# Kernel optimization log

Hardware: AMD Instinct MI355X
Metric: run time of the kernel (lower is better)

The kernel has to match this reference:

```python
import jax, jax.numpy as jnp
import numpy as np

B, L, V, E, H = 64, 256, 256, 256, 1024

def setup_inputs() -> dict:
    key = jax.random.key(0)
    ks = jax.random.split(key, 7)
    inputs = jax.random.randint(ks[0], (B, L), 0, V, dtype=jnp.int32)
    embedding = jax.random.normal(ks[1], (V, E), dtype=jnp.float32)  # stddev=1.0 per emb_init
    # GRU weights: input projections (no bias) and hidden projections (with bias),
    # concatenated over gates [r, z, n].
    Wi = jax.random.normal(ks[2], (E, 3 * H), dtype=jnp.float32) / np.sqrt(E)
    Wh = jax.random.normal(ks[3], (H, 3 * H), dtype=jnp.float32) / np.sqrt(H)
    bh = jnp.zeros((3 * H,), dtype=jnp.float32)
    # Output dense (xavier_uniform-like scale)
    lim = np.sqrt(6.0 / (H + V))
    Wout = jax.random.uniform(ks[4], (H, V), dtype=jnp.float32, minval=-lim, maxval=lim)
    bout = jax.random.normal(ks[5], (V,), dtype=jnp.float32) * 1e-6
    return {"inputs": inputs, "embedding": embedding, "Wi": Wi, "Wh": Wh,
            "bh": bh, "Wout": Wout, "bout": bout}

def reference(inputs, embedding, Wi, Wh, bh, Wout, bout):
    # Embedding lookup: [B, L] -> [B, L, E]
    x = jnp.take(embedding, inputs, axis=0)
    # Precompute input-side gate projections for all timesteps (batched GEMM).
    xw = jnp.einsum('ble,ef->blf', x, Wi)  # [B, L, 3H]
    hidden = Wh.shape[0]

    def step(h, xw_t):
        gh = h @ Wh + bh                       # [B, 3H]
        xr, xz, xn = jnp.split(xw_t, 3, axis=-1)
        hr, hz, hn = jnp.split(gh, 3, axis=-1)
        r = jax.nn.sigmoid(xr + hr)
        z = jax.nn.sigmoid(xz + hz)
        n = jnp.tanh(xn + r * hn)
        h_new = (1.0 - z) * n + z * h          # GRUCell update
        return h_new, h_new

    h0 = jnp.zeros((x.shape[0], hidden), dtype=x.dtype)
    _, ys = jax.lax.scan(step, h0, jnp.swapaxes(xw, 0, 1))  # scan over time
    y = jnp.swapaxes(ys, 0, 1)                 # [B, L, H]
    logits = jnp.einsum('blh,hv->blv', y, Wout) + bout
    return logits
```

## Files before the change

### kernel.cpp

```cpp
#include <hip/hip_runtime.h>
#include <cstdint>
#include <math.h>

#define B_  64
#define L_  256
#define V_  256
#define E_  256
#define H_  1024
#define H3  3072

typedef __bf16 bf16x8 __attribute__((ext_vector_type(8)));
typedef float  f32x4  __attribute__((ext_vector_type(4)));

__device__ __forceinline__ unsigned short f2bf(float f) {
    union { float f; unsigned u; } v; v.f = f;
    unsigned r = v.u + 0x7fffu + ((v.u >> 16) & 1u);
    return (unsigned short)(r >> 16);
}
__device__ __forceinline__ float bf2f(unsigned short u) {
    union { unsigned u; float f; } v; v.u = ((unsigned)u) << 16;
    return v.f;
}

__device__ __forceinline__ int chunk_ok(bf16x8 v) {
    union { bf16x8 b; unsigned u[4]; } cv; cv.b = v;
    int ok = 1;
#pragma unroll
    for (int i = 0; i < 4; i++) {
        unsigned x = cv.u[i] ^ 0xAAAAAAAAu;
        ok &= (int)((x & 0xFFFFu) != 0u) & (int)((x >> 16) != 0u);
    }
    return ok;
}

__global__ __launch_bounds__(256) void prep_transpose_tiled(const float* __restrict__ src,
                                                            unsigned short* __restrict__ dst,
                                                            int rows, int cols) {
    __shared__ unsigned short tile[32][34];
    int n0 = blockIdx.x * 32;
    int k0 = blockIdx.y * 32;
    int tx = threadIdx.x & 31, ty = threadIdx.x >> 5;
#pragma unroll
    for (int j = 0; j < 32; j += 8) {
        float v = src[(size_t)(k0 + ty + j) * cols + (n0 + tx)];
        tile[tx][ty + j] = f2bf(v);
    }
    __syncthreads();
#pragma unroll
    for (int j = 0; j < 32; j += 8)
        dst[(size_t)(n0 + ty + j) * rows + (k0 + tx)] = tile[ty + j][tx];
}

__global__ __launch_bounds__(256) void poison_hist(uint4* __restrict__ p) {
    size_t T = (size_t)blockIdx.x * 256 + threadIdx.x;
    uint4 v; v.x = v.y = v.z = v.w = 0xAAAAAAAAu;
#pragma unroll
    for (int k = 0; k < 4; k++) p[T + (size_t)k * 524288] = v;
}

__global__ void prep_misc(const float* __restrict__ emb,
                          unsigned short* __restrict__ embB,
                          unsigned short* __restrict__ h0b) {
    int idx = blockIdx.x * 256 + threadIdx.x;
    embB[idx] = f2bf(emb[idx]);
    h0b[idx]  = 0;
}

__global__ __launch_bounds__(256, 1) void gru_persistent(
        unsigned short* __restrict__ hist,
        const unsigned short* __restrict__ WhT,
        const unsigned short* __restrict__ WiT,
        const unsigned short* __restrict__ embB,
        const int* __restrict__ tokens,
        const float* __restrict__ bh,
        unsigned short* __restrict__ yB) {
    __shared__ f32x4 red[2][4][6][64];

    int bid = blockIdx.x;
    int btile = bid & 3;
    int jtile = bid >> 2;
    int wave = threadIdx.x >> 6, lane = threadIdx.x & 63;
    int l16 = lane & 15, q = lane >> 4;
    int b0 = btile * 16, j0 = jtile * 16;
    int kbase = wave * 256;

    bf16x8 Wreg[3][8];
#pragma unroll
    for (int g = 0; g < 3; g++) {
        const bf16x8* Brow = (const bf16x8*)(WhT + (size_t)(g * H_ + j0 + l16) * H_);
#pragma unroll
        for (int kk = 0; kk < 8; kk++) {
            Wreg[g][kk] = Brow[(kbase >> 3) + kk * 4 + q];
            asm volatile("" : "+v"(Wreg[g][kk]));
        }
    }
    bf16x8 Wxreg[3][2];
#pragma unroll
    for (int g = 0; g < 3; g++) {
        const bf16x8* Bx = (const bf16x8*)(WiT + (size_t)(g * H_ + j0 + l16) * E_);
#pragma unroll
        for (int c = 0; c < 2; c++) {
            Wxreg[g][c] = Bx[wave * 8 + c * 4 + q];
            asm volatile("" : "+v"(Wxreg[g][c]));
        }
    }

    int Lp  = threadIdx.x & 63;
    int reg = threadIdx.x >> 6;
    int b_local = (Lp >> 4) * 4 + reg;
    int j_local = Lp & 15;
    int b = b0 + b_local, jg = j0 + j_local;
    float bhr = bh[jg];
    float bhz = bh[H_ + jg];
    float bhn = bh[2 * H_ + jg];
    asm volatile("" : "+v"(bhr), "+v"(bhz), "+v"(bhn));
    float hreg = 0.0f;

    const int tokrow = (b0 + l16) * L_;

    for (int t = 0; t < L_; t++) {
        const unsigned short* hist_t  = hist + (size_t)t * (B_ * H_);
        unsigned short*       hist_t1 = hist + (size_t)(t + 1) * (B_ * H_);

        int tok = tokens[tokrow + t];
        const bf16x8* Ax = (const bf16x8*)(embB + (size_t)tok * E_);
        bf16x8 ax0 = Ax[wave * 8 + q];
        bf16x8 ax1 = Ax[wave * 8 + 4 + q];
        f32x4 xacc[3] = {};
#pragma unroll
        for (int g = 0; g < 3; g++) {
            xacc[g] = __builtin_amdgcn_mfma_f32_16x16x32_bf16(ax0, Wxreg[g][0], xacc[g], 0, 0, 0);
            xacc[g] = __builtin_amdgcn_mfma_f32_16x16x32_bf16(ax1, Wxreg[g][1], xacc[g], 0, 0, 0);
        }

        const unsigned short* p = hist_t + (size_t)(b0 + l16) * H_ + kbase + q * 8;
        bf16x8 a0, a1, a2, a3, a4, a5, a6, a7;
        while (true) {
            asm volatile("global_load_dwordx4 %0, %1, off sc0 sc1" : "=v"(a0) : "v"(p));
            asm volatile("global_load_dwordx4 %0, %1, off sc0 sc1" : "=v"(a1) : "v"(p + 32));
            asm volatile("global_load_dwordx4 %0, %1, off sc0 sc1" : "=v"(a2) : "v"(p + 64));
            asm volatile("global_load_dwordx4 %0, %1, off sc0 sc1" : "=v"(a3) : "v"(p + 96));
            asm volatile("global_load_dwordx4 %0, %1, off sc0 sc1" : "=v"(a4) : "v"(p + 128));
            asm volatile("global_load_dwordx4 %0, %1, off sc0 sc1" : "=v"(a5) : "v"(p + 160));
            asm volatile("global_load_dwordx4 %0, %1, off sc0 sc1" : "=v"(a6) : "v"(p + 192));
            asm volatile("global_load_dwordx4 %0, %1, off sc0 sc1" : "=v"(a7) : "v"(p + 224));
            asm volatile("s_waitcnt vmcnt(0)"
                         : "+v"(a0), "+v"(a1), "+v"(a2), "+v"(a3),
                           "+v"(a4), "+v"(a5), "+v"(a6), "+v"(a7)
                         :: "memory");
            int ok = chunk_ok(a0) & chunk_ok(a1) & chunk_ok(a2) & chunk_ok(a3)
                   & chunk_ok(a4) & chunk_ok(a5) & chunk_ok(a6) & chunk_ok(a7);
            if (__all(ok)) break;
            __builtin_amdgcn_s_sleep(1);
        }

        f32x4 acc[3] = {};
#pragma unroll
        for (int g = 0; g < 3; g++) {
            acc[g] = __builtin_amdgcn_mfma_f32_16x16x32_bf16(a0, Wreg[g][0], acc[g], 0, 0, 0);
            acc[g] = __builtin_amdgcn_mfma_f32_16x16x32_bf16(a1, Wreg[g][1], acc[g], 0, 0, 0);
            acc[g] = __builtin_amdgcn_mfma_f32_16x16x32_bf16(a2, Wreg[g][2], acc[g], 0, 0, 0);
            acc[g] = __builtin_amdgcn_mfma_f32_16x16x32_bf16(a3, Wreg[g][3], acc[g], 0, 0, 0);
            acc[g] = __builtin_amdgcn_mfma_f32_16x16x32_bf16(a4, Wreg[g][4], acc[g], 0, 0, 0);
            acc[g] = __builtin_amdgcn_mfma_f32_16x16x32_bf16(a5, Wreg[g][5], acc[g], 0, 0, 0);
            acc[g] = __builtin_amdgcn_mfma_f32_16x16x32_bf16(a6, Wreg[g][6], acc[g], 0, 0, 0);
            acc[g] = __builtin_amdgcn_mfma_f32_16x16x32_bf16(a7, Wreg[g][7], acc[g], 0, 0, 0);
        }

        int par = t & 1;
#pragma unroll
        for (int g = 0; g < 3; g++) {
            red[par][wave][g][lane]     = acc[g];
            red[par][wave][3 + g][lane] = xacc[g];
        }
        __syncthreads();

        float gh0 = red[par][0][0][Lp][reg] + red[par][1][0][Lp][reg] + red[par][2][0][Lp][reg] + red[par][3][0][Lp][reg];
        float gh1 = red[par][0][1][Lp][reg] + red[par][1][1][Lp][reg] + red[par][2][1][Lp][reg] + red[par][3][1][Lp][reg];
        float gh2 = red[par][0][2][Lp][reg] + red[par][1][2][Lp][reg] + red[par][2][2][Lp][reg] + red[par][3][2][Lp][reg];
        float xr  = red[par][0][3][Lp][reg] + red[par][1][3][Lp][reg] + red[par][2][3][Lp][reg] + red[par][3][3][Lp][reg];
        float xz  = red[par][0][4][Lp][reg] + red[par][1][4][Lp][reg] + red[par][2][4][Lp][reg] + red[par][3][4][Lp][reg];
        float xn  = red[par][0][5][Lp][reg] + red[par][1][5][Lp][reg] + red[par][2][5][Lp][reg] + red[par][3][5][Lp][reg];

        float r = 1.0f / (1.0f + __expf(-(xr + gh0 + bhr)));
        float z = 1.0f / (1.0f + __expf(-(xz + gh1 + bhz)));
        float n = tanhf(xn + r * (gh2 + bhn));
        float hnew = (1.0f - z) * n + z * hreg;
        hreg = hnew;

        unsigned short hbv = f2bf(hnew);
        if (hbv == 0xAAAAu) hbv = 0xAAABu;

        {
            unsigned short* hp = hist_t1 + (size_t)b * H_ + jg;
            unsigned hv32 = hbv;
            asm volatile("global_store_short %0, %1, off sc0 sc1"
                         :: "v"(hp), "v"(hv32) : "memory");
        }
        yB[((size_t)b * L_ + t) * H_ + jg] = hbv;
    }
}

__global__ __launch_bounds__(256) void out_gemm(const unsigned short* __restrict__ yB,
                                                const unsigned short* __restrict__ WoutT,
                                                const float* __restrict__ bout,
                                                float* __restrict__ out) {
    int ntile = blockIdx.x;
    int mtile = blockIdx.y;
    int wave = threadIdx.x >> 6, lane = threadIdx.x & 63;
    int l16 = lane & 15, q = lane >> 4;

    int m = mtile * 64 + wave * 16 + l16;
    const bf16x8* Arow = (const bf16x8*)(yB + (size_t)m * H_);
    int n0 = ntile * 64;

    f32x4 acc[4] = {};
    for (int k0 = 0; k0 < H_; k0 += 32) {
        bf16x8 a = Arow[(k0 >> 3) + q];
#pragma unroll
        for (int j = 0; j < 4; j++) {
            const bf16x8* Brow = (const bf16x8*)(WoutT + (size_t)(n0 + j*16 + l16) * H_);
            bf16x8 b = Brow[(k0 >> 3) + q];
            acc[j] = __builtin_amdgcn_mfma_f32_16x16x32_bf16(a, b, acc[j], 0, 0, 0);
        }
    }
    int mrow = mtile * 64 + wave * 16 + q * 4;
#pragma unroll
    for (int j = 0; j < 4; j++) {
        int n = n0 + j * 16 + l16;
        float bias = bout[n];
#pragma unroll
        for (int r = 0; r < 4; r++)
            out[(size_t)(mrow + r) * V_ + n] = acc[j][r] + bias;
    }
}

extern "C" void kernel_launch(void* const* d_in, const int* in_sizes, int n_in,
                              void* d_out, int out_size, void* d_ws, size_t ws_size,
                              hipStream_t stream) {
    const int*   tokens = (const int*)  d_in[0];
    const float* emb    = (const float*)d_in[1];
    const float* Wi     = (const float*)d_in[2];
    const float* Wh     = (const float*)d_in[3];
    const float* bh     = (const float*)d_in[4];
    const float* Wout   = (const float*)d_in[5];
    const float* bout   = (const float*)d_in[6];
    float* out = (float*)d_out;

    char* ws = (char*)d_ws;
    size_t off = 0;
    auto alloc = [&](size_t bytes) -> void* {
        void* p = ws + off;
        off += (bytes + 255) & ~(size_t)255;
        return p;
    };
    unsigned short* WhT   = (unsigned short*)alloc((size_t)H3 * H_ * 2);
    unsigned short* WiT   = (unsigned short*)alloc((size_t)H3 * E_ * 2);
    unsigned short* WoutT = (unsigned short*)alloc((size_t)V_ * H_ * 2);
    unsigned short* embB  = (unsigned short*)alloc((size_t)V_ * E_ * 2);
    unsigned short* yB    = (unsigned short*)alloc((size_t)B_ * L_ * H_ * 2);
    unsigned short* hist  = (unsigned short*)alloc((size_t)(L_ + 1) * B_ * H_ * 2);

    prep_transpose_tiled<<<dim3(H3 / 32, H_ / 32), 256, 0, stream>>>(Wh, WhT, H_, H3);
    prep_transpose_tiled<<<dim3(H3 / 32, E_ / 32), 256, 0, stream>>>(Wi, WiT, E_, H3);
    prep_transpose_tiled<<<dim3(V_ / 32, H_ / 32), 256, 0, stream>>>(Wout, WoutT, H_, V_);
    poison_hist<<<2048, 256, 0, stream>>>((uint4*)(hist + (size_t)B_ * H_));
    prep_misc<<<(V_ * E_) / 256, 256, 0, stream>>>(emb, embB, hist);

    {
        unsigned short* ah = hist;
        const unsigned short* aW = WhT; const unsigned short* aWx = WiT;
        const unsigned short* ae = embB; const int* at = tokens;
        const float* ab = bh; unsigned short* ay = yB;
        void* args[] = {&ah, &aW, &aWx, &ae, &at, &ab, &ay};
        hipLaunchCooperativeKernel((void*)gru_persistent, dim3(256), dim3(256),
                                   args, 0, stream);
    }

    out_gemm<<<dim3(4, 256), 256, 0, stream>>>(yB, WoutT, bout, out);
}
```

Before: 992.9 us.

## Replace poisoned history polling with per-block step flags and double-buffered hidden state

Drops the full per-timestep hidden-state history and the kernel that filled it with a poison pattern. In their place come two ping-pong hidden buffers and per-block progress flags. After storing its hidden slice, each block drains its stores, syncs and publishes its step counter; before reading, wave 0 spins until all 64 column blocks in its batch group have reached the step. This removes the large poison write and the repeated poll-and-validate reloads of the history. In exchange it adds a store drain, an extra block barrier and a flag round trip to each step's critical path, and the spin has a timeout that could silently break ordering.

New measurement: 1.053 ms. 1.06x slower.

```diff
diff --git a/kernel.cpp b/kernel.cpp
--- a/kernel.cpp
+++ b/kernel.cpp
@@ -16,21 +16,6 @@
     union { float f; unsigned u; } v; v.f = f;
     unsigned r = v.u + 0x7fffu + ((v.u >> 16) & 1u);
     return (unsigned short)(r >> 16);
-}
-__device__ __forceinline__ float bf2f(unsigned short u) {
-    union { unsigned u; float f; } v; v.u = ((unsigned)u) << 16;
-    return v.f;
-}
-
-__device__ __forceinline__ int chunk_ok(bf16x8 v) {
-    union { bf16x8 b; unsigned u[4]; } cv; cv.b = v;
-    int ok = 1;
-#pragma unroll
-    for (int i = 0; i < 4; i++) {
-        unsigned x = cv.u[i] ^ 0xAAAAAAAAu;
-        ok &= (int)((x & 0xFFFFu) != 0u) & (int)((x >> 16) != 0u);
-    }
-    return ok;
 }
 
 __global__ __launch_bounds__(256) void prep_transpose_tiled(const float* __restrict__ src,
@@ -51,29 +36,26 @@
         dst[(size_t)(n0 + ty + j) * rows + (k0 + tx)] = tile[ty + j][tx];
 }
 
-__global__ __launch_bounds__(256) void poison_hist(uint4* __restrict__ p) {
-    size_t T = (size_t)blockIdx.x * 256 + threadIdx.x;
-    uint4 v; v.x = v.y = v.z = v.w = 0xAAAAAAAAu;
-#pragma unroll
-    for (int k = 0; k < 4; k++) p[T + (size_t)k * 524288] = v;
-}
-
 __global__ void prep_misc(const float* __restrict__ emb,
                           unsigned short* __restrict__ embB,
-                          unsigned short* __restrict__ h0b) {
+                          unsigned short* __restrict__ h0b,
+                          unsigned* __restrict__ flags) {
     int idx = blockIdx.x * 256 + threadIdx.x;
     embB[idx] = f2bf(emb[idx]);
     h0b[idx]  = 0;
+    if (idx < 4096) flags[idx] = 0;
 }
 
 __global__ __launch_bounds__(256, 1) void gru_persistent(
-        unsigned short* __restrict__ hist,
+        unsigned short* __restrict__ hbuf0,
+        unsigned short* __restrict__ hbuf1,
         const unsigned short* __restrict__ WhT,
         const unsigned short* __restrict__ WiT,
         const unsigned short* __restrict__ embB,
         const int* __restrict__ tokens,
         const float* __restrict__ bh,
-        unsigned short* __restrict__ yB) {
+        unsigned short* __restrict__ yB,
+        unsigned* __restrict__ flagp) {
     __shared__ f32x4 red[2][4][6][64];
 
     int bid = blockIdx.x;
@@ -83,6 +65,9 @@
     int l16 = lane & 15, q = lane >> 4;
     int b0 = btile * 16, j0 = jtile * 16;
     int kbase = wave * 256;
+
+    unsigned* grpflags = flagp + (btile << 10);
+    unsigned* myflag   = grpflags + (jtile << 4);
 
     bf16x8 Wreg[3][8];
 #pragma unroll
@@ -118,9 +103,11 @@
 
     const int tokrow = (b0 + l16) * L_;
 
+    unsigned short* hcur = hbuf0;
+    unsigned short* hnxt = hbuf1;
+
     for (int t = 0; t < L_; t++) {
-        const unsigned short* hist_t  = hist + (size_t)t * (B_ * H_);
-        unsigned short*       hist_t1 = hist + (size_t)(t + 1) * (B_ * H_);
+        int par = t & 1;
 
         int tok = tokens[tokrow + t];
         const bf16x8* Ax = (const bf16x8*)(embB + (size_t)tok * E_);
@@ -133,26 +120,36 @@
             xacc[g] = __builtin_amdgcn_mfma_f32_16x16x32_bf16(ax1, Wxreg[g][1], xacc[g], 0, 0, 0);
         }
 
-        const unsigned short* p = hist_t + (size_t)(b0 + l16) * H_ + kbase + q * 8;
+        if (t > 0) {
+            if (wave == 0) {
+                unsigned tgt = (unsigned)t;
+                int spins = 0;
+                while (true) {
+                    unsigned f = __hip_atomic_load(grpflags + (lane << 4),
+                                                   __ATOMIC_RELAXED,
+                                                   __HIP_MEMORY_SCOPE_AGENT);
+                    if (__all((int)(f >= tgt))) break;
+                    if (++spins > (1 << 20)) break;
+                    __builtin_amdgcn_s_sleep(1);
+                }
+            }
+            __syncthreads();
+        }
+
+        const unsigned short* p = hcur + (size_t)(b0 + l16) * H_ + kbase + q * 8;
         bf16x8 a0, a1, a2, a3, a4, a5, a6, a7;
-        while (true) {
-            asm volatile("global_load_dwordx4 %0, %1, off sc0 sc1" : "=v"(a0) : "v"(p));
-            asm volatile("global_load_dwordx4 %0, %1, off sc0 sc1" : "=v"(a1) : "v"(p + 32));
-            asm volatile("global_load_dwordx4 %0, %1, off sc0 sc1" : "=v"(a2) : "v"(p + 64));
-            asm volatile("global_load_dwordx4 %0, %1, off sc0 sc1" : "=v"(a3) : "v"(p + 96));
-            asm volatile("global_load_dwordx4 %0, %1, off sc0 sc1" : "=v"(a4) : "v"(p + 128));
-            asm volatile("global_load_dwordx4 %0, %1, off sc0 sc1" : "=v"(a5) : "v"(p + 160));
-            asm volatile("global_load_dwordx4 %0, %1, off sc0 sc1" : "=v"(a6) : "v"(p + 192));
-            asm volatile("global_load_dwordx4 %0, %1, off sc0 sc1" : "=v"(a7) : "v"(p + 224));
-            asm volatile("s_waitcnt vmcnt(0)"
-                         : "+v"(a0), "+v"(a1), "+v"(a2), "+v"(a3),
-                           "+v"(a4), "+v"(a5), "+v"(a6), "+v"(a7)
-                         :: "memory");
-            int ok = chunk_ok(a0) & chunk_ok(a1) & chunk_ok(a2) & chunk_ok(a3)
-                   & chunk_ok(a4) & chunk_ok(a5) & chunk_ok(a6) & chunk_ok(a7);
-            if (__all(ok)) break;
-            __builtin_amdgcn_s_sleep(1);
-        }
+        asm volatile("global_load_dwordx4 %0, %1, off sc0 sc1" : "=v"(a0) : "v"(p));
+        asm volatile("global_load_dwordx4 %0, %1, off sc0 sc1" : "=v"(a1) : "v"(p + 32));
+        asm volatile("global_load_dwordx4 %0, %1, off sc0 sc1" : "=v"(a2) : "v"(p + 64));
+        asm volatile("global_load_dwordx4 %0, %1, off sc0 sc1" : "=v"(a3) : "v"(p + 96));
+        asm volatile("global_load_dwordx4 %0, %1, off sc0 sc1" : "=v"(a4) : "v"(p + 128));
+        asm volatile("global_load_dwordx4 %0, %1, off sc0 sc1" : "=v"(a5) : "v"(p + 160));
+        asm volatile("global_load_dwordx4 %0, %1, off sc0 sc1" : "=v"(a6) : "v"(p + 192));
+        asm volatile("global_load_dwordx4 %0, %1, off sc0 sc1" : "=v"(a7) : "v"(p + 224));
+        asm volatile("s_waitcnt vmcnt(0)"
+                     : "+v"(a0), "+v"(a1), "+v"(a2), "+v"(a3),
+                       "+v"(a4), "+v"(a5), "+v"(a6), "+v"(a7)
+                     :: "memory");
 
         f32x4 acc[3] = {};
 #pragma unroll
@@ -166,8 +163,6 @@
             acc[g] = __builtin_amdgcn_mfma_f32_16x16x32_bf16(a6, Wreg[g][6], acc[g], 0, 0, 0);
             acc[g] = __builtin_amdgcn_mfma_f32_16x16x32_bf16(a7, Wreg[g][7], acc[g], 0, 0, 0);
         }
-
-        int par = t & 1;
 #pragma unroll
         for (int g = 0; g < 3; g++) {
             red[par][wave][g][lane]     = acc[g];
@@ -189,15 +184,22 @@
         hreg = hnew;
 
         unsigned short hbv = f2bf(hnew);
-        if (hbv == 0xAAAAu) hbv = 0xAAABu;
-
         {
-            unsigned short* hp = hist_t1 + (size_t)b * H_ + jg;
+            unsigned short* hp = hnxt + (size_t)b * H_ + jg;
             unsigned hv32 = hbv;
             asm volatile("global_store_short %0, %1, off sc0 sc1"
                          :: "v"(hp), "v"(hv32) : "memory");
         }
+        asm volatile("s_waitcnt vmcnt(0)" ::: "memory");
+        __syncthreads();
+
+        if (threadIdx.x == 0)
+            __hip_atomic_store(myflag, (unsigned)(t + 1), __ATOMIC_RELAXED,
+                               __HIP_MEMORY_SCOPE_AGENT);
+
         yB[((size_t)b * L_ + t) * H_ + jg] = hbv;
+
+        unsigned short* tmp = hcur; hcur = hnxt; hnxt = tmp;
     }
 }
 
@@ -259,22 +261,28 @@
     unsigned short* WoutT = (unsigned short*)alloc((size_t)V_ * H_ * 2);
     unsigned short* embB  = (unsigned short*)alloc((size_t)V_ * E_ * 2);
     unsigned short* yB    = (unsigned short*)alloc((size_t)B_ * L_ * H_ * 2);
-    unsigned short* hist  = (unsigned short*)alloc((size_t)(L_ + 1) * B_ * H_ * 2);
+    unsigned short* hb0   = (unsigned short*)alloc((size_t)B_ * H_ * 2);
+    unsigned short* hb1   = (unsigned short*)alloc((size_t)B_ * H_ * 2);
+    unsigned*       flags = (unsigned*)alloc(4096 * sizeof(unsigned));
 
     prep_transpose_tiled<<<dim3(H3 / 32, H_ / 32), 256, 0, stream>>>(Wh, WhT, H_, H3);
     prep_transpose_tiled<<<dim3(H3 / 32, E_ / 32), 256, 0, stream>>>(Wi, WiT, E_, H3);
     prep_transpose_tiled<<<dim3(V_ / 32, H_ / 32), 256, 0, stream>>>(Wout, WoutT, H_, V_);
-    poison_hist<<<2048, 256, 0, stream>>>((uint4*)(hist + (size_t)B_ * H_));
-    prep_misc<<<(V_ * E_) / 256, 256, 0, stream>>>(emb, embB, hist);
+    prep_misc<<<(V_ * E_) / 256, 256, 0, stream>>>(emb, embB, hb0, flags);
 
     {
-        unsigned short* ah = hist;
+        unsigned short* a0 = hb0; unsigned short* a1 = hb1;
         const unsigned short* aW = WhT; const unsigned short* aWx = WiT;
         const unsigned short* ae = embB; const int* at = tokens;
         const float* ab = bh; unsigned short* ay = yB;
-        void* args[] = {&ah, &aW, &aWx, &ae, &at, &ab, &ay};
-        hipLaunchCooperativeKernel((void*)gru_persistent, dim3(256), dim3(256),
-                                   args, 0, stream);
+        unsigned* af = flags;
+        void* args[] = {&a0, &a1, &aW, &aWx, &ae, &at, &ab, &ay, &af};
+        hipError_t err = hipLaunchCooperativeKernel((void*)gru_persistent,
+                                                    dim3(256), dim3(256), args, 0, stream);
+        if (err != hipSuccess) {
+            gru_persistent<<<dim3(256), dim3(256), 0, stream>>>(
+                a0, a1, aW, aWx, ae, at, ab, ay, af);
+        }
     }
 
     out_gemm<<<dim3(4, 256), 256, 0, stream>>>(yB, WoutT, bout, out);
```

## Fuse prep kernels and split hidden-state polling to overlap loads with MFMA

Applied to the files above, without the earlier changes.

The five preprocessing launches (three transposes, the poison fill and the misc conversion) become one kernel that dispatches on block index. In the recurrent loop, the spin-wait now polls only the first half of the previous hidden-state chunk. It then issues the second half's loads and runs the first-half MFMAs while those loads are in flight, re-polling the second half only if it is not ready. A spin cap and a non-cooperative launch fallback are added as safety measures, at the cost of extra branches and a loop that can exit on stale data if the cap is hit.

Result: faster. 973.1 us (-2.0%).

```diff
diff --git a/kernel.cpp b/kernel.cpp
--- a/kernel.cpp
+++ b/kernel.cpp
@@ -17,10 +17,6 @@
     unsigned r = v.u + 0x7fffu + ((v.u >> 16) & 1u);
     return (unsigned short)(r >> 16);
 }
-__device__ __forceinline__ float bf2f(unsigned short u) {
-    union { unsigned u; float f; } v; v.u = ((unsigned)u) << 16;
-    return v.f;
-}
 
 __device__ __forceinline__ int chunk_ok(bf16x8 v) {
     union { bf16x8 b; unsigned u[4]; } cv; cv.b = v;
@@ -33,37 +29,38 @@
     return ok;
 }
 
-__global__ __launch_bounds__(256) void prep_transpose_tiled(const float* __restrict__ src,
-                                                            unsigned short* __restrict__ dst,
-                                                            int rows, int cols) {
+__global__ __launch_bounds__(256) void prep_all(
+        const float* __restrict__ Wh, const float* __restrict__ Wi,
+        const float* __restrict__ Wout, const float* __restrict__ emb,
+        unsigned short* __restrict__ WhT, unsigned short* __restrict__ WiT,
+        unsigned short* __restrict__ WoutT, unsigned short* __restrict__ embB,
+        unsigned short* __restrict__ h0b, uint4* __restrict__ poison) {
     __shared__ unsigned short tile[32][34];
-    int n0 = blockIdx.x * 32;
-    int k0 = blockIdx.y * 32;
+    int bid = blockIdx.x;
+    const float* src; unsigned short* dst; int rows, cols, nt, kt;
+    if (bid < 3072)      { src = Wh;   dst = WhT;   rows = H_; cols = H3; nt = bid % 96; kt = bid / 96; }
+    else if (bid < 3840) { int b = bid - 3072; src = Wi;   dst = WiT;   rows = E_; cols = H3; nt = b % 96; kt = b / 96; }
+    else if (bid < 4096) { int b = bid - 3840; src = Wout; dst = WoutT; rows = H_; cols = V_; nt = b % 8;  kt = b / 8; }
+    else if (bid < 4352) {
+        int idx = (bid - 4096) * 256 + threadIdx.x;
+        embB[idx] = f2bf(emb[idx]);
+        h0b[idx]  = 0;
+        return;
+    } else {
+        size_t T = (size_t)(bid - 4352) * 256 + threadIdx.x;
+        uint4 v; v.x = v.y = v.z = v.w = 0xAAAAAAAAu;
+        poison[T] = v;
+        return;
+    }
+    int n0 = nt * 32, k0 = kt * 32;
     int tx = threadIdx.x & 31, ty = threadIdx.x >> 5;
 #pragma unroll
-    for (int j = 0; j < 32; j += 8) {
-        float v = src[(size_t)(k0 + ty + j) * cols + (n0 + tx)];
-        tile[tx][ty + j] = f2bf(v);
-    }
+    for (int j = 0; j < 32; j += 8)
+        tile[tx][ty + j] = f2bf(src[(size_t)(k0 + ty + j) * cols + (n0 + tx)]);
     __syncthreads();
 #pragma unroll
     for (int j = 0; j < 32; j += 8)
         dst[(size_t)(n0 + ty + j) * rows + (k0 + tx)] = tile[ty + j][tx];
-}
-
-__global__ __launch_bounds__(256) void poison_hist(uint4* __restrict__ p) {
-    size_t T = (size_t)blockIdx.x * 256 + threadIdx.x;
-    uint4 v; v.x = v.y = v.z = v.w = 0xAAAAAAAAu;
-#pragma unroll
-    for (int k = 0; k < 4; k++) p[T + (size_t)k * 524288] = v;
-}
-
-__global__ void prep_misc(const float* __restrict__ emb,
-                          unsigned short* __restrict__ embB,
-                          unsigned short* __restrict__ h0b) {
-    int idx = blockIdx.x * 256 + threadIdx.x;
-    embB[idx] = f2bf(emb[idx]);
-    h0b[idx]  = 0;
 }
 
 __global__ __launch_bounds__(256, 1) void gru_persistent(
@@ -135,24 +132,26 @@
 
         const unsigned short* p = hist_t + (size_t)(b0 + l16) * H_ + kbase + q * 8;
         bf16x8 a0, a1, a2, a3, a4, a5, a6, a7;
-        while (true) {
-            asm volatile("global_load_dwordx4 %0, %1, off sc0 sc1" : "=v"(a0) : "v"(p));
-            asm volatile("global_load_dwordx4 %0, %1, off sc0 sc1" : "=v"(a1) : "v"(p + 32));
-            asm volatile("global_load_dwordx4 %0, %1, off sc0 sc1" : "=v"(a2) : "v"(p + 64));
-            asm volatile("global_load_dwordx4 %0, %1, off sc0 sc1" : "=v"(a3) : "v"(p + 96));
-            asm volatile("global_load_dwordx4 %0, %1, off sc0 sc1" : "=v"(a4) : "v"(p + 128));
-            asm volatile("global_load_dwordx4 %0, %1, off sc0 sc1" : "=v"(a5) : "v"(p + 160));
-            asm volatile("global_load_dwordx4 %0, %1, off sc0 sc1" : "=v"(a6) : "v"(p + 192));
-            asm volatile("global_load_dwordx4 %0, %1, off sc0 sc1" : "=v"(a7) : "v"(p + 224));
-            asm volatile("s_waitcnt vmcnt(0)"
-                         : "+v"(a0), "+v"(a1), "+v"(a2), "+v"(a3),
-                           "+v"(a4), "+v"(a5), "+v"(a6), "+v"(a7)
-                         :: "memory");
-            int ok = chunk_ok(a0) & chunk_ok(a1) & chunk_ok(a2) & chunk_ok(a3)
-                   & chunk_ok(a4) & chunk_ok(a5) & chunk_ok(a6) & chunk_ok(a7);
-            if (__all(ok)) break;
-            __builtin_amdgcn_s_sleep(1);
-        }
+
+        {
+            int spins = 0;
+            while (true) {
+                asm volatile("global_load_dwordx4 %0, %1, off sc0 sc1" : "=v"(a0) : "v"(p));
+                asm volatile("global_load_dwordx4 %0, %1, off sc0 sc1" : "=v"(a1) : "v"(p + 32));
+                asm volatile("global_load_dwordx4 %0, %1, off sc0 sc1" : "=v"(a2) : "v"(p + 64));
+                asm volatile("global_load_dwordx4 %0, %1, off sc0 sc1" : "=v"(a3) : "v"(p + 96));
+                asm volatile("s_waitcnt vmcnt(0)"
+                             : "+v"(a0), "+v"(a1), "+v"(a2), "+v"(a3) :: "memory");
+                int ok = chunk_ok(a0) & chunk_ok(a1) & chunk_ok(a2) & chunk_ok(a3);
+                if (__all(ok)) break;
+                if (++spins > (1 << 18)) break;
+                __builtin_amdgcn_s_sleep(1);
+            }
+        }
+        asm volatile("global_load_dwordx4 %0, %1, off sc0 sc1" : "=v"(a4) : "v"(p + 128));
+        asm volatile("global_load_dwordx4 %0, %1, off sc0 sc1" : "=v"(a5) : "v"(p + 160));
+        asm volatile("global_load_dwordx4 %0, %1, off sc0 sc1" : "=v"(a6) : "v"(p + 192));
+        asm volatile("global_load_dwordx4 %0, %1, off sc0 sc1" : "=v"(a7) : "v"(p + 224));
 
         f32x4 acc[3] = {};
 #pragma unroll
@@ -161,6 +160,30 @@
             acc[g] = __builtin_amdgcn_mfma_f32_16x16x32_bf16(a1, Wreg[g][1], acc[g], 0, 0, 0);
             acc[g] = __builtin_amdgcn_mfma_f32_16x16x32_bf16(a2, Wreg[g][2], acc[g], 0, 0, 0);
             acc[g] = __builtin_amdgcn_mfma_f32_16x16x32_bf16(a3, Wreg[g][3], acc[g], 0, 0, 0);
+        }
+
+        asm volatile("s_waitcnt vmcnt(0)"
+                     : "+v"(a4), "+v"(a5), "+v"(a6), "+v"(a7) :: "memory");
+        {
+            int ok = chunk_ok(a4) & chunk_ok(a5) & chunk_ok(a6) & chunk_ok(a7);
+            if (!__all(ok)) {
+                int spins = 0;
+                while (true) {
+                    __builtin_amdgcn_s_sleep(1);
+                    asm volatile("global_load_dwordx4 %0, %1, off sc0 sc1" : "=v"(a4) : "v"(p + 128));
+                    asm volatile("global_load_dwordx4 %0, %1, off sc0 sc1" : "=v"(a5) : "v"(p + 160));
+                    asm volatile("global_load_dwordx4 %0, %1, off sc0 sc1" : "=v"(a6) : "v"(p + 192));
+                    asm volatile("global_load_dwordx4 %0, %1, off sc0 sc1" : "=v"(a7) : "v"(p + 224));
+                    asm volatile("s_waitcnt vmcnt(0)"
+                                 : "+v"(a4), "+v"(a5), "+v"(a6), "+v"(a7) :: "memory");
+                    int ok2 = chunk_ok(a4) & chunk_ok(a5) & chunk_ok(a6) & chunk_ok(a7);
+                    if (__all(ok2)) break;
+                    if (++spins > (1 << 18)) break;
+                }
+            }
+        }
+#pragma unroll
+        for (int g = 0; g < 3; g++) {
             acc[g] = __builtin_amdgcn_mfma_f32_16x16x32_bf16(a4, Wreg[g][4], acc[g], 0, 0, 0);
             acc[g] = __builtin_amdgcn_mfma_f32_16x16x32_bf16(a5, Wreg[g][5], acc[g], 0, 0, 0);
             acc[g] = __builtin_amdgcn_mfma_f32_16x16x32_bf16(a6, Wreg[g][6], acc[g], 0, 0, 0);
@@ -261,11 +284,8 @@
     unsigned short* yB    = (unsigned short*)alloc((size_t)B_ * L_ * H_ * 2);
     unsigned short* hist  = (unsigned short*)alloc((size_t)(L_ + 1) * B_ * H_ * 2);
 
-    prep_transpose_tiled<<<dim3(H3 / 32, H_ / 32), 256, 0, stream>>>(Wh, WhT, H_, H3);
-    prep_transpose_tiled<<<dim3(H3 / 32, E_ / 32), 256, 0, stream>>>(Wi, WiT, E_, H3);
-    prep_transpose_tiled<<<dim3(V_ / 32, H_ / 32), 256, 0, stream>>>(Wout, WoutT, H_, V_);
-    poison_hist<<<2048, 256, 0, stream>>>((uint4*)(hist + (size_t)B_ * H_));
-    prep_misc<<<(V_ * E_) / 256, 256, 0, stream>>>(emb, embB, hist);
+    prep_all<<<12544, 256, 0, stream>>>(Wh, Wi, Wout, emb, WhT, WiT, WoutT,
+                                        embB, hist, (uint4*)(hist + (size_t)B_ * H_));
 
     {
         unsigned short* ah = hist;
@@ -273,8 +293,12 @@
         const unsigned short* ae = embB; const int* at = tokens;
         const float* ab = bh; unsigned short* ay = yB;
         void* args[] = {&ah, &aW, &aWx, &ae, &at, &ab, &ay};
-        hipLaunchCooperativeKernel((void*)gru_persistent, dim3(256), dim3(256),
-                                   args, 0, stream);
+        hipError_t err = hipLaunchCooperativeKernel((void*)gru_persistent,
+                                                    dim3(256), dim3(256), args, 0, stream);
+        if (err != hipSuccess) {
+            gru_persistent<<<dim3(256), dim3(256), 0, stream>>>(
+                ah, aW, aWx, ae, at, ab, ay);
+        }
     }
 
     out_gemm<<<dim3(4, 256), 256, 0, stream>>>(yB, WoutT, bout, out);
```
